# Performance work log

Hardware: AMD Instinct MI355X
Metric: run time of the kernel (lower is better)

## Reference

```python
import jax, jax.numpy as jnp
import numpy as np

EMBED = 2048
T = 2048  # max_seq_length
BATCH = 2  # hardcoded by the module's initial-state shape


def setup_inputs() -> dict:
    key = jax.random.key(0)
    ks = jax.random.split(key, 7)
    s = 0.02
    return {
        "x": jax.random.normal(ks[0], (BATCH, EMBED), dtype=jnp.float32),
        "W_ih": jax.random.normal(ks[1], (4 * EMBED, EMBED), dtype=jnp.float32) * s,
        "W_hh": jax.random.normal(ks[2], (4 * EMBED, EMBED), dtype=jnp.float32) * s,
        "b_ih": jax.random.normal(ks[3], (4 * EMBED,), dtype=jnp.float32) * s,
        "b_hh": jax.random.normal(ks[4], (4 * EMBED,), dtype=jnp.float32) * s,
        "W_out": jax.random.normal(ks[5], (EMBED, EMBED), dtype=jnp.float32) * s,
        "b_out": jax.random.normal(ks[6], (EMBED,), dtype=jnp.float32) * s,
    }


def reference(x, W_ih, W_hh, b_ih, b_hh, W_out, b_out):
    E = x.shape[-1]

    def step(carry, _):
        inp, h, c = carry  # each [B, E]
        gates = inp @ W_ih.T + b_ih + h @ W_hh.T + b_hh  # [B, 4E]
        i, f, g, o = jnp.split(gates, 4, axis=-1)  # PyTorch gate order i,f,g,o
        c_new = jax.nn.sigmoid(f) * c + jax.nn.sigmoid(i) * jnp.tanh(g)
        h_new = jax.nn.sigmoid(o) * jnp.tanh(c_new)
        # output of single-layer LSTM == h_new; it is fed back as next input
        return (h_new, h_new, c_new), h_new

    h0 = jnp.zeros((x.shape[0], E), dtype=x.dtype)
    c0 = jnp.zeros((x.shape[0], E), dtype=x.dtype)
    _, seq = jax.lax.scan(step, (x, h0, c0), None, length=T)  # [T, B, E]

    out = seq @ W_out.T + b_out  # dropout is identity in eval
    return jnp.transpose(out, (1, 0, 2))  # [B, T, E]
```

## Files before the change

kernel.cpp:

```cpp
#include <hip/hip_runtime.h>
#include <hip/hip_fp16.h>
#include <stdint.h>


#define E 2048
#define NBLK 256
#define NTHR 512
#define HLDS_B 2304
#define PLS_STRIDE 20
#define PLS_PAR 640
#define SMEM_MAIN 23680
#define SMEM_PROJ 131072

typedef uint32_t u32;
typedef unsigned long long u64;

__device__ __forceinline__ float sigf(float x){
  return __builtin_amdgcn_rcpf(1.0f + __expf(-x));
}
__device__ __forceinline__ float tanhfast(float x){
  float e = __expf(2.0f * x);
  return 1.0f - 2.0f * __builtin_amdgcn_rcpf(e + 1.0f);
}

#define ROWFMA8(W0, W1, W2, W3, A0, A1) \
  A0 = fmaf(__low2float(W0),  p0.x, A0); A0 = fmaf(__high2float(W0), p0.y, A0); \
  A0 = fmaf(__low2float(W1),  p0.z, A0); A0 = fmaf(__high2float(W1), p0.w, A0); \
  A0 = fmaf(__low2float(W2),  p1.x, A0); A0 = fmaf(__high2float(W2), p1.y, A0); \
  A0 = fmaf(__low2float(W3),  p1.z, A0); A0 = fmaf(__high2float(W3), p1.w, A0); \
  A1 = fmaf(__low2float(W0),  q0.x, A1); A1 = fmaf(__high2float(W0), q0.y, A1); \
  A1 = fmaf(__low2float(W1),  q0.z, A1); A1 = fmaf(__high2float(W1), q0.w, A1); \
  A1 = fmaf(__low2float(W2),  q1.x, A1); A1 = fmaf(__high2float(W2), q1.y, A1); \
  A1 = fmaf(__low2float(W3),  q1.z, A1); A1 = fmaf(__high2float(W3), q1.w, A1);

#define POLLCHK(J, UJ) \
  if (pend & (1 << J)){ \
    if ((u32)(UJ >> 32) == tag){ \
      hlds[cdst[J]] = __uint_as_float((u32)UJ); \
      pend &= ~(1 << J); \
    } \
  }

#define ISSUE8(R0, R1, R2, R3, R4, R5, R6, R7) \
  asm volatile( \
    "global_load_dwordx2 %0, %8, off sc0 sc1\n\t" \
    "global_load_dwordx2 %1, %8, off offset:512 sc0 sc1\n\t" \
    "global_load_dwordx2 %2, %8, off offset:1024 sc0 sc1\n\t" \
    "global_load_dwordx2 %3, %8, off offset:1536 sc0 sc1\n\t" \
    "global_load_dwordx2 %4, %8, off offset:2048 sc0 sc1\n\t" \
    "global_load_dwordx2 %5, %8, off offset:2560 sc0 sc1\n\t" \
    "global_load_dwordx2 %6, %8, off offset:3072 sc0 sc1\n\t" \
    "global_load_dwordx2 %7, %8, off offset:3584 sc0 sc1" \
    : "=&v"(R0), "=&v"(R1), "=&v"(R2), "=&v"(R3), \
      "=&v"(R4), "=&v"(R5), "=&v"(R6), "=&v"(R7) \
    : "v"(src) : "memory")

#define RELOAD(J, UJ, OFS) \
  if (pend & (1 << J)){ \
    asm volatile("global_load_dwordx2 %0, %1, off offset:" OFS " sc0 sc1" \
                 : "=v"(UJ) : "v"(src) : "memory"); \
  }

__global__ void __launch_bounds__(NTHR, 1) lstm_kernel(
    const float* __restrict__ xin, const float* __restrict__ Wih,
    const float* __restrict__ Whh, const float* __restrict__ bih,
    const float* __restrict__ bhh, u64* __restrict__ chk,
    float* __restrict__ seqout)
{
  extern __shared__ char smem[];
  float* hlds = (float*)smem;
  float* pls  = (float*)(smem + 18432);
  float* bias = (float*)(smem + 23552);

  const int tid  = threadIdx.x;
  const int blk  = blockIdx.x;
  const int e0   = blk << 3;
  const int lane = tid & 63;
  const int wv   = tid >> 6;
  const int rg   = lane >> 3;
  const int ksl  = lane & 7;
  const int ks   = (wv << 3) + ksl;
  const int k0   = ks << 5;

  if (tid < 32){
    const int grow = ((tid >> 3) << 11) + e0 + (tid & 7);
    bias[tid] = bih[grow] + bhh[grow];
  }
  for (int i = tid; i < 2 * E; i += NTHR){
    const int b = i >> 11, k = i & 2047;
    hlds[b * HLDS_B + (k >> 5) * 36 + (k & 31)] = xin[i];
  }
  __syncthreads();

  const float* hb0 = hlds + ks * 36;
  const float* hb1 = hlds + HLDS_B + ks * 36;

  __half2 wh[64];
  float acc0[4] = {0.f, 0.f, 0.f, 0.f};
  float acc1[4] = {0.f, 0.f, 0.f, 0.f};
  #pragma unroll
  for (int rr = 0; rr < 4; ++rr){
    const int row  = (rg << 2) + rr;
    const int grow = ((row >> 3) << 11) + e0 + (row & 7);
    const float* pa = Wih + (size_t)grow * E + k0;
    const float* pb = Whh + (size_t)grow * E + k0;
    #pragma unroll
    for (int c = 0; c < 8; ++c){
      float4 a = *(const float4*)(pa + (c << 2));
      float4 b = *(const float4*)(pb + (c << 2));
      wh[(rr << 4) + (c << 1)    ] =
        __halves2half2(__float2half_rn(a.x + b.x), __float2half_rn(a.y + b.y));
      wh[(rr << 4) + (c << 1) + 1] =
        __halves2half2(__float2half_rn(a.z + b.z), __float2half_rn(a.w + b.w));
      float4 x0 = *(const float4*)(hb0 + (c << 2));
      float4 x1 = *(const float4*)(hb1 + (c << 2));
      acc0[rr] = fmaf(a.x, x0.x, acc0[rr]); acc0[rr] = fmaf(a.y, x0.y, acc0[rr]);
      acc0[rr] = fmaf(a.z, x0.z, acc0[rr]); acc0[rr] = fmaf(a.w, x0.w, acc0[rr]);
      acc1[rr] = fmaf(a.x, x1.x, acc1[rr]); acc1[rr] = fmaf(a.y, x1.y, acc1[rr]);
      acc1[rr] = fmaf(a.z, x1.z, acc1[rr]); acc1[rr] = fmaf(a.w, x1.w, acc1[rr]);
    }
  }

  const float br = bias[lane & 31];
  float creg = 0.0f;

  int cdst[8];
  #pragma unroll
  for (int j = 0; j < 8; ++j){
    const int c = (wv << 9) + (j << 6) + lane;
    const int b = (c >> 3) & 1;
    const int e = ((c >> 4) << 3) | (c & 7);
    cdst[j] = b * HLDS_B + (e >> 5) * 36 + (e & 31);
  }
  u64* const pchk0 = chk;
  u64* const pchk1 = chk + 4096;

  for (int t = 0; t < 2048; ++t){
    #pragma unroll
    for (int m = 1; m <= 4; m <<= 1){
      #pragma unroll
      for (int rr = 0; rr < 4; ++rr){
        acc0[rr] += __shfl_xor(acc0[rr], m, 64);
        acc1[rr] += __shfl_xor(acc1[rr], m, 64);
      }
    }
    if (ksl == 0){
      float2* pw = (float2*)(pls + (t & 1) * PLS_PAR);
      #pragma unroll
      for (int rr = 0; rr < 4; ++rr)
        pw[((rg << 2) + rr) * (PLS_STRIDE / 2) + wv] = make_float2(acc0[rr], acc1[rr]);
    }
    __syncthreads();

    if (wv == 0){
      const int r = lane & 31;
      const int b = lane >> 5;
      const float* rp = pls + (t & 1) * PLS_PAR + r * PLS_STRIDE;
      float4 v0 = *(const float4*)(rp);
      float4 v1 = *(const float4*)(rp + 4);
      float4 v2 = *(const float4*)(rp + 8);
      float4 v3 = *(const float4*)(rp + 12);
      float s = br + (b ? (v0.y + v0.w + v1.y + v1.w + v2.y + v2.w + v3.y + v3.w)
                        : (v0.x + v0.z + v1.x + v1.z + v2.x + v2.z + v3.x + v3.z));
      const float gi = s;
      const float gf = __shfl(s, (lane + 8)  & 63, 64);
      const float gg = __shfl(s, (lane + 16) & 63, 64);
      const float go = __shfl(s, (lane + 24) & 63, 64);
      if (r < 8){
        const float cn = sigf(gf) * creg + sigf(gi) * tanhfast(gg);
        const float hn = sigf(go) * tanhfast(cn);
        creg = cn;
        if (t < 2047){
          const u64 pk = ((u64)(u32)(t + 1) << 32) | (u64)__float_as_uint(hn);
          u64* dst = (((t + 1) & 1) ? pchk1 : pchk0) + (blk << 4) + (b << 3) + r;
          asm volatile("global_store_dwordx2 %0, %1, off sc0 sc1"
                       :: "v"(dst), "v"(pk) : "memory");
        }
        seqout[(((size_t)b << 11) + (size_t)t) * E + e0 + r] = hn;
      }
    }
    if (t == 2047) break;

    {
      const u64* src = (((t + 1) & 1) ? pchk1 : pchk0) + (wv << 9) + lane;
      const u32 tag = (u32)(t + 1);
      u64 a0_, a1_, a2_, a3_, a4_, a5_, a6_, a7_;
      ISSUE8(a0_, a1_, a2_, a3_, a4_, a5_, a6_, a7_);
      asm volatile("s_waitcnt vmcnt(0)" ::: "memory");
      int pend = 0xFF;
      while (true){
        POLLCHK(0, a0_) POLLCHK(1, a1_) POLLCHK(2, a2_) POLLCHK(3, a3_)
        POLLCHK(4, a4_) POLLCHK(5, a5_) POLLCHK(6, a6_) POLLCHK(7, a7_)
        if (pend == 0) break;
        RELOAD(0, a0_, "0")    RELOAD(1, a1_, "512")
        RELOAD(2, a2_, "1024") RELOAD(3, a3_, "1536")
        RELOAD(4, a4_, "2048") RELOAD(5, a5_, "2560")
        RELOAD(6, a6_, "3072") RELOAD(7, a7_, "3584")
        __builtin_amdgcn_s_sleep(1);
        asm volatile("s_waitcnt vmcnt(0)" ::: "memory");
      }
      asm volatile("s_waitcnt lgkmcnt(0)" ::: "memory");
      __builtin_amdgcn_sched_barrier(0);
    }

    #pragma unroll
    for (int rr = 0; rr < 4; ++rr){ acc0[rr] = 0.f; acc1[rr] = 0.f; }
    #pragma unroll
    for (int c8 = 0; c8 < 4; ++c8){
      float4 p0 = *(const float4*)(hb0 + (c8 << 3));
      float4 p1 = *(const float4*)(hb0 + (c8 << 3) + 4);
      float4 q0 = *(const float4*)(hb1 + (c8 << 3));
      float4 q1 = *(const float4*)(hb1 + (c8 << 3) + 4);
      #pragma unroll
      for (int rr = 0; rr < 4; ++rr){
        ROWFMA8(wh[(rr << 4) + (c8 << 2)],     wh[(rr << 4) + (c8 << 2) + 1],
                wh[(rr << 4) + (c8 << 2) + 2], wh[(rr << 4) + (c8 << 2) + 3],
                acc0[rr], acc1[rr]);
      }
    }
  }
}

__global__ void __launch_bounds__(512, 1) proj_pair_kernel(
    const float* __restrict__ src, float* __restrict__ io,
    const float* __restrict__ Wout, const float* __restrict__ bout)
{
  extern __shared__ char smem[];
  u32* ah = (u32*)smem;
  const int tid = threadIdx.x;
  const int blk = blockIdx.x;
  const size_t rbase = (size_t)(blk >> 1) * 32 * E;
  const int ch = (blk & 1) << 10;

  for (int idx = tid; idx < 32768; idx += 512){
    const float2 v = *(const float2*)(src + rbase + ((size_t)idx << 1));
    ah[idx] = (u32)__half_as_ushort(__float2half_rn(v.x))
            | ((u32)__half_as_ushort(__float2half_rn(v.y)) << 16);
  }
  __syncthreads();

  const int n0 = ch + tid;
  const int n1 = n0 + 512;
  const float* wr0 = Wout + (size_t)n0 * E;
  const float* wr1 = Wout + (size_t)n1 * E;
  float acc0[32], acc1[32];
  #pragma unroll
  for (int m = 0; m < 32; ++m){ acc0[m] = 0.0f; acc1[m] = 0.0f; }
  for (int kc = 0; kc < 256; ++kc){
    const float4 a0v = *(const float4*)(wr0 + (kc << 3));
    const float4 a1v = *(const float4*)(wr0 + (kc << 3) + 4);
    const float4 b0v = *(const float4*)(wr1 + (kc << 3));
    const float4 b1v = *(const float4*)(wr1 + (kc << 3) + 4);
    const u32* hp = ah + (kc << 2);
    #pragma unroll
    for (int m = 0; m < 32; ++m){
      const uint4 hv = *(const uint4*)(hp + (m << 10));
      const __half2 h0 = __builtin_bit_cast(__half2, hv.x);
      const __half2 h1 = __builtin_bit_cast(__half2, hv.y);
      const __half2 h2 = __builtin_bit_cast(__half2, hv.z);
      const __half2 h3 = __builtin_bit_cast(__half2, hv.w);
      const float x0 = __low2float(h0), x1 = __high2float(h0);
      const float x2 = __low2float(h1), x3 = __high2float(h1);
      const float x4 = __low2float(h2), x5 = __high2float(h2);
      const float x6 = __low2float(h3), x7 = __high2float(h3);
      acc0[m] = fmaf(a0v.x, x0, acc0[m]); acc0[m] = fmaf(a0v.y, x1, acc0[m]);
      acc0[m] = fmaf(a0v.z, x2, acc0[m]); acc0[m] = fmaf(a0v.w, x3, acc0[m]);
      acc0[m] = fmaf(a1v.x, x4, acc0[m]); acc0[m] = fmaf(a1v.y, x5, acc0[m]);
      acc0[m] = fmaf(a1v.z, x6, acc0[m]); acc0[m] = fmaf(a1v.w, x7, acc0[m]);
      acc1[m] = fmaf(b0v.x, x0, acc1[m]); acc1[m] = fmaf(b0v.y, x1, acc1[m]);
      acc1[m] = fmaf(b0v.z, x2, acc1[m]); acc1[m] = fmaf(b0v.w, x3, acc1[m]);
      acc1[m] = fmaf(b1v.x, x4, acc1[m]); acc1[m] = fmaf(b1v.y, x5, acc1[m]);
      acc1[m] = fmaf(b1v.z, x6, acc1[m]); acc1[m] = fmaf(b1v.w, x7, acc1[m]);
    }
  }
  const float bo0 = bout[n0];
  const float bo1 = bout[n1];
  #pragma unroll
  for (int m = 0; m < 32; ++m){
    io[rbase + ((size_t)m << 11) + n0] = acc0[m] + bo0;
    io[rbase + ((size_t)m << 11) + n1] = acc1[m] + bo1;
  }
}

__global__ void __launch_bounds__(256, 1) proj_kernel(
    float* __restrict__ io, const float* __restrict__ Wout,
    const float* __restrict__ bout)
{
  extern __shared__ char smem[];
  float* alds = (float*)smem;
  const int tid = threadIdx.x;
  const size_t rbase = (size_t)blockIdx.x * 16 * E;

  for (int idx = tid; idx < 8192; idx += 256){
    float4 v = *(const float4*)(io + rbase + ((size_t)idx << 2));
    *(float4*)(alds + (idx << 2)) = v;
  }
  __syncthreads();

  for (int p = 0; p < 2; ++p){
    const int n0 = (p << 10) + tid;
    const int n1 = n0 + 256;
    const int n2 = n0 + 512;
    const int n3 = n0 + 768;
    const float* wr0 = Wout + (size_t)n0 * E;
    const float* wr1 = Wout + (size_t)n1 * E;
    const float* wr2 = Wout + (size_t)n2 * E;
    const float* wr3 = Wout + (size_t)n3 * E;
    float acc0[16], acc1[16], acc2[16], acc3[16];
    #pragma unroll
    for (int m = 0; m < 16; ++m){
      acc0[m] = 0.0f; acc1[m] = 0.0f; acc2[m] = 0.0f; acc3[m] = 0.0f;
    }
    for (int kc = 0; kc < 256; ++kc){
      const float4 a0v = *(const float4*)(wr0 + (kc << 3));
      const float4 a1v = *(const float4*)(wr0 + (kc << 3) + 4);
      const float4 b0v = *(const float4*)(wr1 + (kc << 3));
      const float4 b1v = *(const float4*)(wr1 + (kc << 3) + 4);
      const float4 c0v = *(const float4*)(wr2 + (kc << 3));
      const float4 c1v = *(const float4*)(wr2 + (kc << 3) + 4);
      const float4 d0v = *(const float4*)(wr3 + (kc << 3));
      const float4 d1v = *(const float4*)(wr3 + (kc << 3) + 4);
      const float* ap = alds + (kc << 3);
      #pragma unroll
      for (int m = 0; m < 16; ++m){
        const float* a = ap + (m << 11);
        float4 x0 = *(const float4*)(a);
        float4 x1 = *(const float4*)(a + 4);
        acc0[m] = fmaf(a0v.x, x0.x, acc0[m]); acc0[m] = fmaf(a0v.y, x0.y, acc0[m]);
        acc0[m] = fmaf(a0v.z, x0.z, acc0[m]); acc0[m] = fmaf(a0v.w, x0.w, acc0[m]);
        acc0[m] = fmaf(a1v.x, x1.x, acc0[m]); acc0[m] = fmaf(a1v.y, x1.y, acc0[m]);
        acc0[m] = fmaf(a1v.z, x1.z, acc0[m]); acc0[m] = fmaf(a1v.w, x1.w, acc0[m]);
        acc1[m] = fmaf(b0v.x, x0.x, acc1[m]); acc1[m] = fmaf(b0v.y, x0.y, acc1[m]);
        acc1[m] = fmaf(b0v.z, x0.z, acc1[m]); acc1[m] = fmaf(b0v.w, x0.w, acc1[m]);
        acc1[m] = fmaf(b1v.x, x1.x, acc1[m]); acc1[m] = fmaf(b1v.y, x1.y, acc1[m]);
        acc1[m] = fmaf(b1v.z, x1.z, acc1[m]); acc1[m] = fmaf(b1v.w, x1.w, acc1[m]);
        acc2[m] = fmaf(c0v.x, x0.x, acc2[m]); acc2[m] = fmaf(c0v.y, x0.y, acc2[m]);
        acc2[m] = fmaf(c0v.z, x0.z, acc2[m]); acc2[m] = fmaf(c0v.w, x0.w, acc2[m]);
        acc2[m] = fmaf(c1v.x, x1.x, acc2[m]); acc2[m] = fmaf(c1v.y, x1.y, acc2[m]);
        acc2[m] = fmaf(c1v.z, x1.z, acc2[m]); acc2[m] = fmaf(c1v.w, x1.w, acc2[m]);
        acc3[m] = fmaf(d0v.x, x0.x, acc3[m]); acc3[m] = fmaf(d0v.y, x0.y, acc3[m]);
        acc3[m] = fmaf(d0v.z, x0.z, acc3[m]); acc3[m] = fmaf(d0v.w, x0.w, acc3[m]);
        acc3[m] = fmaf(d1v.x, x1.x, acc3[m]); acc3[m] = fmaf(d1v.y, x1.y, acc3[m]);
        acc3[m] = fmaf(d1v.z, x1.z, acc3[m]); acc3[m] = fmaf(d1v.w, x1.w, acc3[m]);
      }
    }
    const float bo0 = bout[n0];
    const float bo1 = bout[n1];
    const float bo2 = bout[n2];
    const float bo3 = bout[n3];
    #pragma unroll
    for (int m = 0; m < 16; ++m){
      io[rbase + ((size_t)m << 11) + n0] = acc0[m] + bo0;
      io[rbase + ((size_t)m << 11) + n1] = acc1[m] + bo1;
      io[rbase + ((size_t)m << 11) + n2] = acc2[m] + bo2;
      io[rbase + ((size_t)m << 11) + n3] = acc3[m] + bo3;
    }
  }
}

extern "C" void kernel_launch(void* const* d_in, const int* in_sizes, int n_in,
                              void* d_out, int out_size, void* d_ws, size_t ws_size,
                              hipStream_t stream)
{
  const float* xin  = (const float*)d_in[0];
  const float* Wih  = (const float*)d_in[1];
  const float* Whh  = (const float*)d_in[2];
  const float* bih  = (const float*)d_in[3];
  const float* bhh  = (const float*)d_in[4];
  const float* Wout = (const float*)d_in[5];
  const float* bout = (const float*)d_in[6];
  float* out = (float*)d_out;

  u64* chk = (u64*)d_ws;
  const size_t SEQ_BYTES = (size_t)2 * 2048 * E * sizeof(float);
  const bool big = ws_size >= 65536 + SEQ_BYTES;
  float* seqdst = big ? (float*)((char*)d_ws + 65536) : out;

  hipFuncSetAttribute((const void*)lstm_kernel,
                      hipFuncAttributeMaxDynamicSharedMemorySize, SMEM_MAIN);
  hipFuncSetAttribute((const void*)proj_pair_kernel,
                      hipFuncAttributeMaxDynamicSharedMemorySize, SMEM_PROJ);
  hipFuncSetAttribute((const void*)proj_kernel,
                      hipFuncAttributeMaxDynamicSharedMemorySize, SMEM_PROJ);

  void* args[] = { (void*)&xin, (void*)&Wih, (void*)&Whh, (void*)&bih, (void*)&bhh,
                   (void*)&chk, (void*)&seqdst };
  hipLaunchCooperativeKernel((const void*)lstm_kernel, dim3(NBLK), dim3(NTHR),
                             args, SMEM_MAIN, stream);

  if (big){
    proj_pair_kernel<<<256, 512, SMEM_PROJ, stream>>>(seqdst, out, Wout, bout);
  } else {
    proj_kernel<<<256, 256, SMEM_PROJ, stream>>>(out, Wout, bout);
  }
}
```

Baseline: 8.069 ms.

## Pack both batch h values into dwordx4 flags, fp16 dot2 projection, fused gate activation

Measured after the change: 7.714 ms. -4.4%, faster.

```diff
diff --git a/kernel.cpp b/kernel.cpp
--- a/kernel.cpp
+++ b/kernel.cpp
@@ -14,6 +14,8 @@
 
 typedef uint32_t u32;
 typedef unsigned long long u64;
+typedef unsigned int u32x4 __attribute__((ext_vector_type(4)));
+typedef _Float16 hf2 __attribute__((ext_vector_type(2)));
 
 __device__ __forceinline__ float sigf(float x){
   return __builtin_amdgcn_rcpf(1.0f + __expf(-x));
@@ -21,6 +23,14 @@
 __device__ __forceinline__ float tanhfast(float x){
   float e = __expf(2.0f * x);
   return 1.0f - 2.0f * __builtin_amdgcn_rcpf(e + 1.0f);
+}
+__device__ __forceinline__ u32 f16p(float lo, float hi){
+  return (u32)__half_as_ushort(__float2half_rn(lo))
+       | ((u32)__half_as_ushort(__float2half_rn(hi)) << 16);
+}
+__device__ __forceinline__ float dot2(u32 a, u32 b, float acc){
+  return __builtin_amdgcn_fdot2(__builtin_bit_cast(hf2, a),
+                                __builtin_bit_cast(hf2, b), acc, false);
 }
 
 #define ROWFMA8(W0, W1, W2, W3, A0, A1) \
@@ -33,38 +43,33 @@
   A1 = fmaf(__low2float(W2),  q1.x, A1); A1 = fmaf(__high2float(W2), q1.y, A1); \
   A1 = fmaf(__low2float(W3),  q1.z, A1); A1 = fmaf(__high2float(W3), q1.w, A1);
 
-#define POLLCHK(J, UJ) \
-  if (pend & (1 << J)){ \
-    if ((u32)(UJ >> 32) == tag){ \
-      hlds[cdst[J]] = __uint_as_float((u32)UJ); \
-      pend &= ~(1 << J); \
-    } \
-  }
-
-#define ISSUE8(R0, R1, R2, R3, R4, R5, R6, R7) \
+#define CHKQ(J, QJ) \
+  if (pend & (1 << (2*(J)))){ \
+    if ((QJ).y == tag){ \
+      hlds[cd0[J]] = __uint_as_float((QJ).x); pend &= ~(1 << (2*(J))); } } \
+  if (pend & (2 << (2*(J)))){ \
+    if ((QJ).w == tag){ \
+      hlds[cd1[J]] = __uint_as_float((QJ).z); pend &= ~(2 << (2*(J))); } }
+
+#define ISSUE4Q(Q0, Q1, Q2, Q3) \
   asm volatile( \
-    "global_load_dwordx2 %0, %8, off sc0 sc1\n\t" \
-    "global_load_dwordx2 %1, %8, off offset:512 sc0 sc1\n\t" \
-    "global_load_dwordx2 %2, %8, off offset:1024 sc0 sc1\n\t" \
-    "global_load_dwordx2 %3, %8, off offset:1536 sc0 sc1\n\t" \
-    "global_load_dwordx2 %4, %8, off offset:2048 sc0 sc1\n\t" \
-    "global_load_dwordx2 %5, %8, off offset:2560 sc0 sc1\n\t" \
-    "global_load_dwordx2 %6, %8, off offset:3072 sc0 sc1\n\t" \
-    "global_load_dwordx2 %7, %8, off offset:3584 sc0 sc1" \
-    : "=&v"(R0), "=&v"(R1), "=&v"(R2), "=&v"(R3), \
-      "=&v"(R4), "=&v"(R5), "=&v"(R6), "=&v"(R7) \
+    "global_load_dwordx4 %0, %4, off sc0 sc1\n\t" \
+    "global_load_dwordx4 %1, %4, off offset:1024 sc0 sc1\n\t" \
+    "global_load_dwordx4 %2, %4, off offset:2048 sc0 sc1\n\t" \
+    "global_load_dwordx4 %3, %4, off offset:3072 sc0 sc1" \
+    : "=&v"(Q0), "=&v"(Q1), "=&v"(Q2), "=&v"(Q3) \
     : "v"(src) : "memory")
 
-#define RELOAD(J, UJ, OFS) \
-  if (pend & (1 << J)){ \
-    asm volatile("global_load_dwordx2 %0, %1, off offset:" OFS " sc0 sc1" \
-                 : "=v"(UJ) : "v"(src) : "memory"); \
+#define RELOADQ(J, QJ, OFS) \
+  if (pend & (3 << (2*(J)))){ \
+    asm volatile("global_load_dwordx4 %0, %1, off offset:" OFS " sc0 sc1" \
+                 : "=v"(QJ) : "v"(src) : "memory"); \
   }
 
 __global__ void __launch_bounds__(NTHR, 1) lstm_kernel(
     const float* __restrict__ xin, const float* __restrict__ Wih,
     const float* __restrict__ Whh, const float* __restrict__ bih,
-    const float* __restrict__ bhh, u64* __restrict__ chk,
+    const float* __restrict__ bhh, u32x4* __restrict__ chk16,
     float* __restrict__ seqout)
 {
   extern __shared__ char smem[];
@@ -124,16 +129,13 @@
   const float br = bias[lane & 31];
   float creg = 0.0f;
 
-  int cdst[8];
-  #pragma unroll
-  for (int j = 0; j < 8; ++j){
-    const int c = (wv << 9) + (j << 6) + lane;
-    const int b = (c >> 3) & 1;
-    const int e = ((c >> 4) << 3) | (c & 7);
-    cdst[j] = b * HLDS_B + (e >> 5) * 36 + (e & 31);
-  }
-  u64* const pchk0 = chk;
-  u64* const pchk1 = chk + 4096;
+  int cd0[4], cd1[4];
+  #pragma unroll
+  for (int j = 0; j < 4; ++j){
+    const int e = (wv << 8) + (j << 6) + lane;
+    cd0[j] = (e >> 5) * 36 + (e & 31);
+    cd1[j] = HLDS_B + cd0[j];
+  }
 
   for (int t = 0; t < 2048; ++t){
     #pragma unroll
@@ -162,18 +164,24 @@
       float4 v3 = *(const float4*)(rp + 12);
       float s = br + (b ? (v0.y + v0.w + v1.y + v1.w + v2.y + v2.w + v3.y + v3.w)
                         : (v0.x + v0.z + v1.x + v1.z + v2.x + v2.z + v3.x + v3.z));
-      const float gi = s;
-      const float gf = __shfl(s, (lane + 8)  & 63, 64);
-      const float gg = __shfl(s, (lane + 16) & 63, 64);
-      const float go = __shfl(s, (lane + 24) & 63, 64);
+      const int g = r >> 3;
+      const float arg = (g == 2) ? (s + s) : s;
+      const float t0v = sigf(arg);
+      const float nl  = (g == 2) ? (2.0f * t0v - 1.0f) : t0v;
+      const float SF = __shfl(nl, (lane + 8)  & 63, 64);
+      const float TG = __shfl(nl, (lane + 16) & 63, 64);
+      const float SO = __shfl(nl, (lane + 24) & 63, 64);
       if (r < 8){
-        const float cn = sigf(gf) * creg + sigf(gi) * tanhfast(gg);
-        const float hn = sigf(go) * tanhfast(cn);
+        const float cn = SF * creg + nl * TG;
+        const float hn = SO * tanhfast(cn);
         creg = cn;
-        if (t < 2047){
-          const u64 pk = ((u64)(u32)(t + 1) << 32) | (u64)__float_as_uint(hn);
-          u64* dst = (((t + 1) & 1) ? pchk1 : pchk0) + (blk << 4) + (b << 3) + r;
-          asm volatile("global_store_dwordx2 %0, %1, off sc0 sc1"
+        const u32 h32 = __float_as_uint(hn);
+        const u32 oth = (u32)__shfl((int)h32, (lane + 32) & 63, 64);
+        if (t < 2047 && b == 0){
+          const u32 tg = (u32)(t + 1);
+          u32x4 pk; pk.x = h32; pk.y = tg; pk.z = oth; pk.w = tg;
+          u32x4* dst = chk16 + (((t + 1) & 1) << 11) + e0 + lane;
+          asm volatile("global_store_dwordx4 %0, %1, off sc0 sc1"
                        :: "v"(dst), "v"(pk) : "memory");
         }
         seqout[(((size_t)b << 11) + (size_t)t) * E + e0 + r] = hn;
@@ -182,20 +190,18 @@
     if (t == 2047) break;
 
     {
-      const u64* src = (((t + 1) & 1) ? pchk1 : pchk0) + (wv << 9) + lane;
+      const u32x4* src = (const u32x4*)chk16 + (((t + 1) & 1) << 11)
+                       + (wv << 8) + lane;
       const u32 tag = (u32)(t + 1);
-      u64 a0_, a1_, a2_, a3_, a4_, a5_, a6_, a7_;
-      ISSUE8(a0_, a1_, a2_, a3_, a4_, a5_, a6_, a7_);
+      u32x4 q0, q1, q2, q3;
+      ISSUE4Q(q0, q1, q2, q3);
       asm volatile("s_waitcnt vmcnt(0)" ::: "memory");
       int pend = 0xFF;
       while (true){
-        POLLCHK(0, a0_) POLLCHK(1, a1_) POLLCHK(2, a2_) POLLCHK(3, a3_)
-        POLLCHK(4, a4_) POLLCHK(5, a5_) POLLCHK(6, a6_) POLLCHK(7, a7_)
+        CHKQ(0, q0) CHKQ(1, q1) CHKQ(2, q2) CHKQ(3, q3)
         if (pend == 0) break;
-        RELOAD(0, a0_, "0")    RELOAD(1, a1_, "512")
-        RELOAD(2, a2_, "1024") RELOAD(3, a3_, "1536")
-        RELOAD(4, a4_, "2048") RELOAD(5, a5_, "2560")
-        RELOAD(6, a6_, "3072") RELOAD(7, a7_, "3584")
+        RELOADQ(0, q0, "0")    RELOADQ(1, q1, "1024")
+        RELOADQ(2, q2, "2048") RELOADQ(3, q3, "3072")
         __builtin_amdgcn_s_sleep(1);
         asm volatile("s_waitcnt vmcnt(0)" ::: "memory");
       }
@@ -221,9 +227,20 @@
   }
 }
 
-__global__ void __launch_bounds__(512, 1) proj_pair_kernel(
+__global__ void wout_cvt(const float* __restrict__ w, u32* __restrict__ o)
+{
+  const size_t i = (((size_t)blockIdx.x << 8) + threadIdx.x) << 3;
+  float4 a = *(const float4*)(w + i);
+  float4 b = *(const float4*)(w + i + 4);
+  uint4 r;
+  r.x = f16p(a.x, a.y); r.y = f16p(a.z, a.w);
+  r.z = f16p(b.x, b.y); r.w = f16p(b.z, b.w);
+  *(uint4*)(o + (i >> 1)) = r;
+}
+
+__global__ void __launch_bounds__(512, 1) proj_pair16(
     const float* __restrict__ src, float* __restrict__ io,
-    const float* __restrict__ Wout, const float* __restrict__ bout)
+    const u32* __restrict__ wf, const float* __restrict__ bout)
 {
   extern __shared__ char smem[];
   u32* ah = (u32*)smem;
@@ -234,8 +251,57 @@
 
   for (int idx = tid; idx < 32768; idx += 512){
     const float2 v = *(const float2*)(src + rbase + ((size_t)idx << 1));
-    ah[idx] = (u32)__half_as_ushort(__float2half_rn(v.x))
-            | ((u32)__half_as_ushort(__float2half_rn(v.y)) << 16);
+    ah[idx] = f16p(v.x, v.y);
+  }
+  __syncthreads();
+
+  const int n0 = ch + tid;
+  const int n1 = n0 + 512;
+  const u32* wr0 = wf + (size_t)n0 * 1024;
+  const u32* wr1 = wf + (size_t)n1 * 1024;
+  float acc0[32], acc1[32];
+  #pragma unroll
+  for (int m = 0; m < 32; ++m){ acc0[m] = 0.0f; acc1[m] = 0.0f; }
+  for (int kc = 0; kc < 256; ++kc){
+    const uint4 wa = *(const uint4*)(wr0 + (kc << 2));
+    const uint4 wb = *(const uint4*)(wr1 + (kc << 2));
+    const u32* hp = ah + (kc << 2);
+    #pragma unroll
+    for (int m = 0; m < 32; ++m){
+      const uint4 hv = *(const uint4*)(hp + (m << 10));
+      acc0[m] = dot2(wa.x, hv.x, acc0[m]);
+      acc0[m] = dot2(wa.y, hv.y, acc0[m]);
+      acc0[m] = dot2(wa.z, hv.z, acc0[m]);
+      acc0[m] = dot2(wa.w, hv.w, acc0[m]);
+      acc1[m] = dot2(wb.x, hv.x, acc1[m]);
+      acc1[m] = dot2(wb.y, hv.y, acc1[m]);
+      acc1[m] = dot2(wb.z, hv.z, acc1[m]);
+      acc1[m] = dot2(wb.w, hv.w, acc1[m]);
+    }
+  }
+  const float bo0 = bout[n0];
+  const float bo1 = bout[n1];
+  #pragma unroll
+  for (int m = 0; m < 32; ++m){
+    io[rbase + ((size_t)m << 11) + n0] = acc0[m] + bo0;
+    io[rbase + ((size_t)m << 11) + n1] = acc1[m] + bo1;
+  }
+}
+
+__global__ void __launch_bounds__(512, 1) proj_pair_kernel(
+    const float* __restrict__ src, float* __restrict__ io,
+    const float* __restrict__ Wout, const float* __restrict__ bout)
+{
+  extern __shared__ char smem[];
+  u32* ah = (u32*)smem;
+  const int tid = threadIdx.x;
+  const int blk = blockIdx.x;
+  const size_t rbase = (size_t)(blk >> 1) * 32 * E;
+  const int ch = (blk & 1) << 10;
+
+  for (int idx = tid; idx < 32768; idx += 512){
+    const float2 v = *(const float2*)(src + rbase + ((size_t)idx << 1));
+    ah[idx] = f16p(v.x, v.y);
   }
   __syncthreads();
 
@@ -371,24 +437,35 @@
   const float* bout = (const float*)d_in[6];
   float* out = (float*)d_out;
 
-  u64* chk = (u64*)d_ws;
+  u32x4* chk16 = (u32x4*)d_ws;
   const size_t SEQ_BYTES = (size_t)2 * 2048 * E * sizeof(float);
-  const bool big = ws_size >= 65536 + SEQ_BYTES;
+  const size_t WF_BYTES  = (size_t)E * E * 2;
+  const bool big  = ws_size >= 65536 + SEQ_BYTES;
+  const bool big2 = ws_size >= 65536 + SEQ_BYTES + WF_BYTES;
   float* seqdst = big ? (float*)((char*)d_ws + 65536) : out;
+  u32*   wf     = (u32*)((char*)d_ws + 65536 + SEQ_BYTES);
 
   hipFuncSetAttribute((const void*)lstm_kernel,
                       hipFuncAttributeMaxDynamicSharedMemorySize, SMEM_MAIN);
+  hipFuncSetAttribute((const void*)proj_pair16,
+                      hipFuncAttributeMaxDynamicSharedMemorySize, SMEM_PROJ);
   hipFuncSetAttribute((const void*)proj_pair_kernel,
                       hipFuncAttributeMaxDynamicSharedMemorySize, SMEM_PROJ);
   hipFuncSetAttribute((const void*)proj_kernel,
                       hipFuncAttributeMaxDynamicSharedMemorySize, SMEM_PROJ);
 
+  if (big2){
+    wout_cvt<<<2048, 256, 0, stream>>>(Wout, wf);
+  }
+
   void* args[] = { (void*)&xin, (void*)&Wih, (void*)&Whh, (void*)&bih, (void*)&bhh,
-                   (void*)&chk, (void*)&seqdst };
+                   (void*)&chk16, (void*)&seqdst };
   hipLaunchCooperativeKernel((const void*)lstm_kernel, dim3(NBLK), dim3(NTHR),
                              args, SMEM_MAIN, stream);
 
-  if (big){
+  if (big2){
+    proj_pair16<<<256, 512, SMEM_PROJ, stream>>>(seqdst, out, wf, bout);
+  } else if (big){
     proj_pair_kernel<<<256, 512, SMEM_PROJ, stream>>>(seqdst, out, Wout, bout);
   } else {
     proj_kernel<<<256, 256, SMEM_PROJ, stream>>>(out, Wout, bout);
```
